# Kernel tuning notes

Measured on AMD Instinct MI355X. Metric: run time of the kernel, lower is better.

The kernel has to match this reference:

```python
import jax, jax.numpy as jnp
import numpy as np

N_EMBD = 768
N_HEAD = 12
HEAD_DIM = N_EMBD // N_HEAD
B = 4
L_MAIN = 1024
L_SIDE = 1024
HALF = L_SIDE // 2  # occurrences of each modality per row
LN_EPS = 1e-5


def setup_inputs() -> dict:
    key = jax.random.key(0)
    ks = jax.random.split(key, 16)
    x = jax.random.normal(ks[0], (B, L_MAIN, N_EMBD), jnp.float32)
    # ages in years, sorted per-row (events arrive in time order), all >= 0
    age = jnp.sort(jax.random.uniform(ks[1], (B, L_MAIN), jnp.float32) * 80.0, axis=1)
    mod_age = jnp.sort(jax.random.uniform(ks[2], (B, L_SIDE), jnp.float32) * 80.0, axis=1)
    # each row holds exactly HALF tokens of modality 2 and HALF of modality 3, randomly interleaved
    base = jnp.concatenate([jnp.full((HALF,), 2, jnp.int32), jnp.full((HALF,), 3, jnp.int32)])
    mod_idx = jax.vmap(lambda k: jax.random.permutation(k, base))(jax.random.split(ks[3], B))
    mod2_emb = jax.random.normal(ks[4], (B * HALF, N_EMBD), jnp.float32)
    mod3_emb = jax.random.normal(ks[5], (B * HALF, N_EMBD), jnp.float32)

    def lin(k, fan_out, fan_in):
        return 0.02 * jax.random.normal(k, (fan_out, fan_in), jnp.float32)

    params = dict(
        ln0_w=jnp.ones((N_EMBD,), jnp.float32), ln0_b=jnp.zeros((N_EMBD,), jnp.float32),
        ln1_w=jnp.ones((N_EMBD,), jnp.float32), ln1_b=jnp.zeros((N_EMBD,), jnp.float32),
        ln2_w=jnp.ones((N_EMBD,), jnp.float32), ln2_b=jnp.zeros((N_EMBD,), jnp.float32),
        q_w=lin(ks[6], N_EMBD, N_EMBD), q_b=jnp.zeros((N_EMBD,), jnp.float32),
        k_w=lin(ks[7], N_EMBD, N_EMBD), k_b=jnp.zeros((N_EMBD,), jnp.float32),
        v_w=lin(ks[8], N_EMBD, N_EMBD), v_b=jnp.zeros((N_EMBD,), jnp.float32),
        c_w=lin(ks[9], N_EMBD, N_EMBD), c_b=jnp.zeros((N_EMBD,), jnp.float32),
        fc_w=lin(ks[10], 4 * N_EMBD, N_EMBD), fc_b=jnp.zeros((4 * N_EMBD,), jnp.float32),
        proj_w=lin(ks[11], N_EMBD, 4 * N_EMBD), proj_b=jnp.zeros((N_EMBD,), jnp.float32),
    )
    return dict(x=x, age=age, mod_idx=mod_idx, mod_age=mod_age,
                mod2_emb=mod2_emb, mod3_emb=mod3_emb, **params)


def _ln(t, w, b):
    m = jnp.mean(t, axis=-1, keepdims=True)
    v = jnp.var(t, axis=-1, keepdims=True)
    return (t - m) * jax.lax.rsqrt(v + LN_EPS) * w + b


def _fuse_embed(mod_idx, mod_age, mod2_emb, mod3_emb):
    # torch: stable argsort by age, then scatter each modality's embeddings into
    # its matching positions in row-major nonzero order.
    order = jnp.argsort(mod_age, axis=1, stable=True)
    s_idx = jnp.take_along_axis(mod_idx, order, axis=1)  # [B, L_side]
    rows = jnp.arange(s_idx.shape[0])[:, None]
    def scatter_mod(val, m_emb):
        mask = s_idx == val
        occ = jnp.cumsum(mask, axis=1) - 1          # per-row occurrence counter
        gidx = rows * HALF + jnp.clip(occ, 0, HALF - 1)  # global row-major index
        return jnp.where(mask[..., None], m_emb[gidx], 0.0)
    return scatter_mod(2, mod2_emb) + scatter_mod(3, mod3_emb)


def _cross_fusion(x, age, mod_idx, mod_age, mod2_emb, mod3_emb,
                  ln0_w, ln0_b, ln1_w, ln1_b, ln2_w, ln2_b,
                  q_w, q_b, k_w, k_b, v_w, v_b, c_w, c_b,
                  fc_w, fc_b, proj_w, proj_b):
    mod_x = _fuse_embed(mod_idx, mod_age, mod2_emb, mod3_emb)  # [B, L_side, E]
    # time_attention_mask: query may attend to keys with key_age <= query_age, pad = key_age >= 0
    attn_mask = (age[:, :, None] >= mod_age[:, None, :]) & (mod_age >= 0.0)[:, None, :]
    attn_mask = attn_mask[:, None, :, :]  # [B, 1, L_main, L_side]

    xn = _ln(x, ln1_w, ln1_b)
    sn = _ln(mod_x, ln0_w, ln0_b)
    q = (xn @ q_w.T + q_b).reshape(B, L_MAIN, N_HEAD, HEAD_DIM).transpose(0, 2, 1, 3)
    k = (sn @ k_w.T + k_b).reshape(B, L_SIDE, N_HEAD, HEAD_DIM).transpose(0, 2, 1, 3)
    v = (sn @ v_w.T + v_b).reshape(B, L_SIDE, N_HEAD, HEAD_DIM).transpose(0, 2, 1, 3)

    att = jnp.einsum('bhqd,bhkd->bhqk', q, k) * (HEAD_DIM ** -0.5)
    all_masked = ~jnp.any(attn_mask, axis=-1, keepdims=True)
    # fully-masked rows: use 0 logits (uniform softmax) then zero out -> matches
    # torch's masked_fill(all_masked, 0) after nan softmax, but grad-safe.
    neg = jnp.where(all_masked, 0.0, -jnp.inf)
    att = jnp.where(attn_mask, att, neg)
    att = jax.nn.softmax(att, axis=-1)
    att = jnp.where(all_masked, 0.0, att)

    y = jnp.einsum('bhqk,bhkd->bhqd', att, v)
    y = y.transpose(0, 2, 1, 3).reshape(B, L_MAIN, N_EMBD)
    x = x + (y @ c_w.T + c_b)
    h = _ln(x, ln2_w, ln2_b)
    h = jax.nn.gelu(h @ fc_w.T + fc_b, approximate=False)
    x = x + (h @ proj_w.T + proj_b)
    return x


def reference(x, age, mod_idx, mod_age, mod2_emb, mod3_emb,
              ln0_w, ln0_b, ln1_w, ln1_b, ln2_w, ln2_b,
              q_w, q_b, k_w, k_b, v_w, v_b, c_w, c_b,
              fc_w, fc_b, proj_w, proj_b):
    return _cross_fusion(x, age, mod_idx, mod_age, mod2_emb, mod3_emb,
                         ln0_w, ln0_b, ln1_w, ln1_b, ln2_w, ln2_b,
                         q_w, q_b, k_w, k_b, v_w, v_b, c_w, c_b,
                         fc_w, fc_b, proj_w, proj_b)
```

## Files before the change

### kernel.cpp

```cpp
#include <hip/hip_runtime.h>

#define N_EMBD 768
#define SEQ    1024
#define NBATCH 4
#define NHEAD  12
#define HDIM   64
#define NROWS  4096
#define FFN    3072
#define W768   589824
#define WFC    2359296
#define NCVT   6912

typedef unsigned short u16;
typedef __bf16 bf16x8 __attribute__((ext_vector_type(8)));
typedef float  f32x4  __attribute__((ext_vector_type(4)));
typedef unsigned short u16x8 __attribute__((ext_vector_type(8)));

typedef const __attribute__((address_space(1))) unsigned int gu32;
typedef __attribute__((address_space(3))) unsigned int lu32;
#define GLL(g, l) __builtin_amdgcn_global_load_lds((gu32*)(g), (lu32*)(l), 16, 0, 0)

__device__ __forceinline__ u16 f2bf(float f) {
    union { float f; unsigned int i; } v; v.f = f;
    unsigned int r = v.i + 0x7fffu + ((v.i >> 16) & 1u);
    return (u16)(r >> 16);
}

__global__ __launch_bounds__(256) void prep_kernel(const float* __restrict__ qw,
                                                   const float* __restrict__ kw,
                                                   const float* __restrict__ vw,
                                                   const float* __restrict__ cw,
                                                   const float* __restrict__ fcw,
                                                   const float* __restrict__ pw,
                                                   u16* __restrict__ wdst,
                                                   const float* __restrict__ x,
                                                   const float* __restrict__ ln1w,
                                                   const float* __restrict__ ln1b,
                                                   u16* __restrict__ xn,
                                                   const int* __restrict__ mod_idx,
                                                   int* __restrict__ g) {
    int bx = blockIdx.x;
    if (bx < NCVT) {
        size_t e = ((size_t)bx * 256 + threadIdx.x) * 4;
        const float* src; size_t base;
        if      (e < 1 * (size_t)W768) { src = qw;  base = 0; }
        else if (e < 2 * (size_t)W768) { src = kw;  base = 1 * (size_t)W768; }
        else if (e < 3 * (size_t)W768) { src = vw;  base = 2 * (size_t)W768; }
        else if (e < 4 * (size_t)W768) { src = cw;  base = 3 * (size_t)W768; }
        else if (e < 4 * (size_t)W768 + WFC) { src = fcw; base = 4 * (size_t)W768; }
        else { src = pw; base = 4 * (size_t)W768 + WFC; }
        float4 v = *(const float4*)(src + (e - base));
        ushort4 o;
        o.x = f2bf(v.x); o.y = f2bf(v.y); o.z = f2bf(v.z); o.w = f2bf(v.w);
        *(ushort4*)(wdst + e) = o;
    } else if (bx < NCVT + 1024) {
        int row  = (bx - NCVT) * 4 + (threadIdx.x >> 6);
        int lane = threadIdx.x & 63;
        const float* p = x + (size_t)row * N_EMBD;
        float vals[12];
        float s = 0.f, sq = 0.f;
#pragma unroll
        for (int c = 0; c < 12; c++) {
            float v = p[c * 64 + lane];
            vals[c] = v; s += v; sq += v * v;
        }
#pragma unroll
        for (int o = 32; o > 0; o >>= 1) { s += __shfl_xor(s, o); sq += __shfl_xor(sq, o); }
        float mean = s * (1.0f / 768.0f);
        float var  = sq * (1.0f / 768.0f) - mean * mean;
        float r    = rsqrtf(var + 1e-5f);
        u16* d = xn + (size_t)row * N_EMBD;
#pragma unroll
        for (int c = 0; c < 12; c++) {
            int idx = c * 64 + lane;
            d[idx] = f2bf((vals[c] - mean) * r * ln1w[idx] + ln1b[idx]);
        }
    } else {
        __shared__ int sc[256];
        int b = bx - NCVT - 1024;
        int j = threadIdx.x;
        int4 mi = *(const int4*)(mod_idx + b * SEQ + j * 4);
        int f0 = (mi.x == 2), f1 = (mi.y == 2), f2v = (mi.z == 2), f3 = (mi.w == 2);
        int t1 = f0 + f1, t2 = t1 + f2v, t3 = t2 + f3;
        sc[j] = t3;
        __syncthreads();
        for (int off = 1; off < 256; off <<= 1) {
            int add = (j >= off) ? sc[j - off] : 0;
            __syncthreads();
            sc[j] += add;
            __syncthreads();
        }
        int excl = sc[j] - t3;
        int cin[4] = {excl + f0, excl + t1, excl + t2, excl + t3};
        int fl[4] = {f0, f1, f2v, f3};
#pragma unroll
        for (int i2 = 0; i2 < 4; i2++) {
            int jj = j * 4 + i2;
            int occ = fl[i2] ? (cin[i2] - 1) : (jj - cin[i2]);
            occ = occ < 0 ? 0 : (occ > 511 ? 511 : occ);
            g[b * SEQ + jj] = fl[i2] ? (b * 512 + occ) : (2048 + b * 512 + occ);
        }
    }
}

__global__ __launch_bounds__(256) void ln_rows(const float* __restrict__ src,
                                               const float* __restrict__ src2,
                                               const int* __restrict__ g,
                                               const float* __restrict__ w,
                                               const float* __restrict__ b,
                                               u16* __restrict__ dst) {
    int row  = blockIdx.x * 4 + (threadIdx.x >> 6);
    int lane = threadIdx.x & 63;
    const float* p;
    if (g) {
        int gi = g[row];
        p = (gi < 2048) ? (src + (size_t)gi * N_EMBD)
                        : (src2 + (size_t)(gi - 2048) * N_EMBD);
    } else {
        p = src + (size_t)row * N_EMBD;
    }
    float vals[12];
    float s = 0.f, sq = 0.f;
#pragma unroll
    for (int c = 0; c < 12; c++) {
        float v = p[c * 64 + lane];
        vals[c] = v; s += v; sq += v * v;
    }
#pragma unroll
    for (int o = 32; o > 0; o >>= 1) { s += __shfl_xor(s, o); sq += __shfl_xor(sq, o); }
    float mean = s * (1.0f / 768.0f);
    float var  = sq * (1.0f / 768.0f) - mean * mean;
    float r    = rsqrtf(var + 1e-5f);
    u16* d = dst + (size_t)row * N_EMBD;
#pragma unroll
    for (int c = 0; c < 12; c++) {
        int idx = c * 64 + lane;
        d[idx] = f2bf((vals[c] - mean) * r * w[idx] + b[idx]);
    }
}

__device__ __forceinline__ void core128(const u16* __restrict__ A, const u16* __restrict__ W,
                                        int K, int m0, int n0, int t,
                                        u16* As, u16* Bs, f32x4 (&acc)[4][4]) {
    int w = t >> 6, lane = t & 63, quad = lane >> 4, l16 = lane & 15;
    int r16 = lane >> 2, c8 = (lane & 3) * 8;
    int wm = (w >> 1) * 64, wn = (w & 1) * 64;
    for (int k0 = 0; k0 < K; k0 += 32) {
        __syncthreads();
        const u16* ga = A + (size_t)(m0 + w * 32 + r16) * K + k0 + c8;
        const u16* gb = W + (size_t)(n0 + w * 32 + r16) * K + k0 + c8;
        GLL(ga,                  &As[(w * 32) * 32]);
        GLL(ga + 16 * (size_t)K, &As[(w * 32 + 16) * 32]);
        GLL(gb,                  &Bs[(w * 32) * 32]);
        GLL(gb + 16 * (size_t)K, &Bs[(w * 32 + 16) * 32]);
        __syncthreads();
        bf16x8 af[4], bfr[4];
#pragma unroll
        for (int i = 0; i < 4; i++)
            af[i] = *(const bf16x8*)&As[(wm + i * 16 + l16) * 32 + quad * 8];
#pragma unroll
        for (int j = 0; j < 4; j++)
            bfr[j] = *(const bf16x8*)&Bs[(wn + j * 16 + l16) * 32 + quad * 8];
#pragma unroll
        for (int i = 0; i < 4; i++)
#pragma unroll
            for (int j = 0; j < 4; j++)
                acc[i][j] = __builtin_amdgcn_mfma_f32_16x16x32_bf16(af[i], bfr[j], acc[i][j], 0, 0, 0);
    }
}

__device__ __forceinline__ void core64(const u16* __restrict__ A, const u16* __restrict__ W,
                                       int K, int kBeg, int kEnd, int m0, int n0, int t,
                                       u16* As, u16* Bs, f32x4 (&acc)[2][4]) {
    int w = t >> 6, lane = t & 63, quad = lane >> 4, l16 = lane & 15;
    int r16 = lane >> 2, c8 = (lane & 3) * 8;
    int wm = (w >> 1) * 32, wn = (w & 1) * 64;
    for (int k0 = kBeg; k0 < kEnd; k0 += 32) {
        __syncthreads();
        const u16* gb = W + (size_t)(n0 + w * 32 + r16) * K + k0 + c8;
        GLL(A + (size_t)(m0 + w * 16 + r16) * K + k0 + c8, &As[(w * 16) * 32]);
        GLL(gb,                  &Bs[(w * 32) * 32]);
        GLL(gb + 16 * (size_t)K, &Bs[(w * 32 + 16) * 32]);
        __syncthreads();
        bf16x8 af[2], bfr[4];
#pragma unroll
        for (int i = 0; i < 2; i++)
            af[i] = *(const bf16x8*)&As[(wm + i * 16 + l16) * 32 + quad * 8];
#pragma unroll
        for (int j = 0; j < 4; j++)
            bfr[j] = *(const bf16x8*)&Bs[(wn + j * 16 + l16) * 32 + quad * 8];
#pragma unroll
        for (int i = 0; i < 2; i++)
#pragma unroll
            for (int j = 0; j < 4; j++)
                acc[i][j] = __builtin_amdgcn_mfma_f32_16x16x32_bf16(af[i], bfr[j], acc[i][j], 0, 0, 0);
    }
}

__global__ __launch_bounds__(256) void gemm_qkv(const u16* __restrict__ xn,
                                                const u16* __restrict__ sn,
                                                const u16* __restrict__ wq,
                                                const float* __restrict__ qb,
                                                const float* __restrict__ kb,
                                                const float* __restrict__ vb,
                                                u16* __restrict__ outbase) {
    __shared__ u16 As[128 * 32], Bs[128 * 32];
    int z = blockIdx.z;
    const u16* A = (z == 0) ? xn : sn;
    const u16* W = wq + (size_t)z * W768;
    const float* bias = (z == 0) ? qb : ((z == 1) ? kb : vb);
    u16* C = outbase + (size_t)z * ((size_t)NROWS * N_EMBD);
    int m0 = blockIdx.y * 128, n0 = blockIdx.x * 128;
    int t = threadIdx.x;
    f32x4 acc[4][4];
#pragma unroll
    for (int i = 0; i < 4; i++)
#pragma unroll
        for (int j = 0; j < 4; j++) acc[i][j] = (f32x4){0.f, 0.f, 0.f, 0.f};
    core128(A, W, N_EMBD, m0, n0, t, As, Bs, acc);
    int w = t >> 6, lane = t & 63, quad = lane >> 4, l16 = lane & 15;
    int wm = (w >> 1) * 64, wn = (w & 1) * 64;
#pragma unroll
    for (int j = 0; j < 4; j++) {
        int col = n0 + wn + j * 16 + l16;
        float bv = bias[col];
#pragma unroll
        for (int i = 0; i < 4; i++) {
            int rowb = m0 + wm + i * 16 + quad * 4;
#pragma unroll
            for (int r = 0; r < 4; r++)
                C[(size_t)(rowb + r) * N_EMBD + col] = f2bf(acc[i][j][r] + bv);
        }
    }
}

__global__ __launch_bounds__(256) void gemm_fc(const u16* __restrict__ A,
                                               const u16* __restrict__ W,
                                               const float* __restrict__ bias,
                                               u16* __restrict__ C) {
    __shared__ u16 As[128 * 32], Bs[128 * 32];
    int m0 = blockIdx.y * 128, n0 = blockIdx.x * 128;
    int t = threadIdx.x;
    f32x4 acc[4][4];
#pragma unroll
    for (int i = 0; i < 4; i++)
#pragma unroll
        for (int j = 0; j < 4; j++) acc[i][j] = (f32x4){0.f, 0.f, 0.f, 0.f};
    core128(A, W, N_EMBD, m0, n0, t, As, Bs, acc);
    int w = t >> 6, lane = t & 63, quad = lane >> 4, l16 = lane & 15;
    int wm = (w >> 1) * 64, wn = (w & 1) * 64;
#pragma unroll
    for (int j = 0; j < 4; j++) {
        int col = n0 + wn + j * 16 + l16;
        float bv = bias[col];
#pragma unroll
        for (int i = 0; i < 4; i++) {
            int rowb = m0 + wm + i * 16 + quad * 4;
#pragma unroll
            for (int r = 0; r < 4; r++) {
                float v = acc[i][j][r] + bv;
                float y = v * (1.595769122f + 0.071354816f * v * v);
                float gel = v / (1.0f + __expf(-y));
                C[(size_t)(rowb + r) * FFN + col] = f2bf(gel);
            }
        }
    }
}

__global__ __launch_bounds__(256) void gemm_cproj(const u16* __restrict__ A,
                                                  const u16* __restrict__ W,
                                                  const float* __restrict__ bias,
                                                  const float* __restrict__ Res,
                                                  float* __restrict__ C) {
    __shared__ u16 As[64 * 32], Bs[128 * 32];
    int m0 = blockIdx.y * 64, n0 = blockIdx.x * 128;
    int t = threadIdx.x;
    f32x4 acc[2][4];
#pragma unroll
    for (int i = 0; i < 2; i++)
#pragma unroll
        for (int j = 0; j < 4; j++) acc[i][j] = (f32x4){0.f, 0.f, 0.f, 0.f};
    core64(A, W, N_EMBD, 0, N_EMBD, m0, n0, t, As, Bs, acc);
    int w = t >> 6, lane = t & 63, quad = lane >> 4, l16 = lane & 15;
    int wm = (w >> 1) * 32, wn = (w & 1) * 64;
#pragma unroll
    for (int j = 0; j < 4; j++) {
        int col = n0 + wn + j * 16 + l16;
        float bv = bias[col];
#pragma unroll
        for (int i = 0; i < 2; i++) {
            int rowb = m0 + wm + i * 16 + quad * 4;
#pragma unroll
            for (int r = 0; r < 4; r++) {
                size_t idx = (size_t)(rowb + r) * N_EMBD + col;
                C[idx] = acc[i][j][r] + bv + Res[idx];
            }
        }
    }
}

__global__ __launch_bounds__(256) void gemm_proj_split(const u16* __restrict__ A,
                                                       const u16* __restrict__ W,
                                                       float* __restrict__ p0,
                                                       float* __restrict__ p1) {
    __shared__ u16 As[64 * 32], Bs[128 * 32];
    int z = blockIdx.z;
    float* P = z ? p1 : p0;
    int m0 = blockIdx.y * 64, n0 = blockIdx.x * 128;
    int t = threadIdx.x;
    f32x4 acc[2][4];
#pragma unroll
    for (int i = 0; i < 2; i++)
#pragma unroll
        for (int j = 0; j < 4; j++) acc[i][j] = (f32x4){0.f, 0.f, 0.f, 0.f};
    core64(A, W, FFN, z * (FFN / 2), (z + 1) * (FFN / 2), m0, n0, t, As, Bs, acc);
    int w = t >> 6, lane = t & 63, quad = lane >> 4, l16 = lane & 15;
    int wm = (w >> 1) * 32, wn = (w & 1) * 64;
#pragma unroll
    for (int j = 0; j < 4; j++) {
        int col = n0 + wn + j * 16 + l16;
#pragma unroll
        for (int i = 0; i < 2; i++) {
            int rowb = m0 + wm + i * 16 + quad * 4;
#pragma unroll
            for (int r = 0; r < 4; r++)
                P[(size_t)(rowb + r) * N_EMBD + col] = acc[i][j][r];
        }
    }
}

__global__ __launch_bounds__(256) void reduce_proj(const float* __restrict__ p0,
                                                   const float* __restrict__ p1,
                                                   const float* __restrict__ bias,
                                                   const float* __restrict__ x1,
                                                   float* __restrict__ out) {
    size_t idx = ((size_t)blockIdx.x * 256 + threadIdx.x) * 4;
    int col = (int)(idx % N_EMBD);
    float4 a = *(const float4*)(p0 + idx);
    float4 b = *(const float4*)(p1 + idx);
    float4 r = *(const float4*)(x1 + idx);
    float4 bb = *(const float4*)(bias + col);
    float4 o;
    o.x = a.x + b.x + r.x + bb.x;
    o.y = a.y + b.y + r.y + bb.y;
    o.z = a.z + b.z + r.z + bb.z;
    o.w = a.w + b.w + r.w + bb.w;
    *(float4*)(out + idx) = o;
}

#define KST 72

__global__ __launch_bounds__(256) void attn_kernel(const u16* __restrict__ Q,
                                                   const u16* __restrict__ K,
                                                   const u16* __restrict__ V,
                                                   const float* __restrict__ age,
                                                   const float* __restrict__ mod_age,
                                                   u16* __restrict__ Y) {
    __shared__ u16 Kl[64 * KST];
    __shared__ u16 Vt[64 * KST];
    __shared__ u16 Pl[4][16 * KST];

    int bx = blockIdx.x;
    int qt = 15 - (bx / 48);
    int bh = bx % 48;
    int b = bh / NHEAD, h = bh % NHEAD;
    int t = threadIdx.x;
    int w = t >> 6, lane = t & 63, quad = lane >> 4, l16 = lane & 15;
    int q0 = qt * 64 + w * 16;

    size_t qrowbase = ((size_t)(b * SEQ + q0 + l16)) * N_EMBD + h * HDIM;
    bf16x8 qf0 = *(const bf16x8*)&Q[qrowbase + quad * 8];
    bf16x8 qf1 = *(const bf16x8*)&Q[qrowbase + 32 + quad * 8];

    float age_r[4];
#pragma unroll
    for (int r = 0; r < 4; r++) age_r[r] = age[b * SEQ + q0 + quad * 4 + r];
    float age_q0      = __shfl(age_r[0], 0);
    float age_max_blk = age[b * SEQ + qt * 64 + 63];
    float mod_min     = mod_age[b * SEQ];

    float mv0 = (lane < 16) ? mod_age[b * SEQ + lane * 64] : 1e30f;
    unsigned long long bm = __ballot(mv0 > age_max_blk);
    int nkt = bm ? (__ffsll(bm) - 1) : 16;

    int krow0 = t >> 3,        kc8 = (t & 7) * 8;
    int krow1 = 32 + (t >> 3);
    int vrow  = t & 63;
    int vc8_0 = t >> 6, vc8_1 = 4 + (t >> 6);

    float m_i[4] = {-1e30f, -1e30f, -1e30f, -1e30f};
    float l_i[4] = {0.f, 0.f, 0.f, 0.f};
    f32x4 o[4];
#pragma unroll
    for (int nt = 0; nt < 4; nt++) o[nt] = (f32x4){0.f, 0.f, 0.f, 0.f};

    u16x8 kr0, kr1, vr0, vr1;
    float mreg = 0.f;
    if (nkt > 0) {
        size_t kb = ((size_t)(b * SEQ)) * N_EMBD + h * HDIM;
        kr0 = *(const u16x8*)(K + kb + (size_t)krow0 * N_EMBD + kc8);
        kr1 = *(const u16x8*)(K + kb + (size_t)krow1 * N_EMBD + kc8);
        vr0 = *(const u16x8*)(V + kb + (size_t)vrow * N_EMBD + vc8_0 * 8);
        vr1 = *(const u16x8*)(V + kb + (size_t)vrow * N_EMBD + vc8_1 * 8);
        mreg = mod_age[b * SEQ + lane];
    }

    for (int kt = 0; kt < nkt; kt++) {
        __syncthreads();
        *(u16x8*)&Kl[krow0 * KST + kc8] = kr0;
        *(u16x8*)&Kl[krow1 * KST + kc8] = kr1;
#pragma unroll
        for (int e = 0; e < 8; e++) Vt[(vc8_0 * 8 + e) * KST + vrow] = vr0[e];
#pragma unroll
        for (int e = 0; e < 8; e++) Vt[(vc8_1 * 8 + e) * KST + vrow] = vr1[e];
        float mcur = mreg;
        __syncthreads();

        if (kt + 1 < nkt) {
            size_t kb = ((size_t)(b * SEQ + (kt + 1) * 64)) * N_EMBD + h * HDIM;
            kr0 = *(const u16x8*)(K + kb + (size_t)krow0 * N_EMBD + kc8);
            kr1 = *(const u16x8*)(K + kb + (size_t)krow1 * N_EMBD + kc8);
            vr0 = *(const u16x8*)(V + kb + (size_t)vrow * N_EMBD + vc8_0 * 8);
            vr1 = *(const u16x8*)(V + kb + (size_t)vrow * N_EMBD + vc8_1 * 8);
            mreg = mod_age[b * SEQ + (kt + 1) * 64 + lane];
        }

        float tile_max = __shfl(mcur, 63);
        bool need_mask = tile_max > age_q0;
        float p[4][4];
#pragma unroll
        for (int jt = 0; jt < 4; jt++) {
            f32x4 s = (f32x4){0.f, 0.f, 0.f, 0.f};
            bf16x8 kf0 = *(const bf16x8*)&Kl[(jt * 16 + l16) * KST + quad * 8];
            bf16x8 kf1 = *(const bf16x8*)&Kl[(jt * 16 + l16) * KST + 32 + quad * 8];
            s = __builtin_amdgcn_mfma_f32_16x16x32_bf16(qf0, kf0, s, 0, 0, 0);
            s = __builtin_amdgcn_mfma_f32_16x16x32_bf16(qf1, kf1, s, 0, 0, 0);
            float mval = __shfl(mcur, jt * 16 + l16);
#pragma unroll
            for (int r = 0; r < 4; r++) {
                float sv = s[r] * 0.125f;
                p[jt][r] = (!need_mask || mval <= age_r[r]) ? sv : -1e30f;
            }
        }
        float alpha[4];
#pragma unroll
        for (int r = 0; r < 4; r++) {
            float mx = fmaxf(fmaxf(p[0][r], p[1][r]), fmaxf(p[2][r], p[3][r]));
#pragma unroll
            for (int msk = 1; msk < 16; msk <<= 1) mx = fmaxf(mx, __shfl_xor(mx, msk));
            float mnew = fmaxf(m_i[r], mx);
            alpha[r] = __expf(m_i[r] - mnew);
            float srow = 0.f;
#pragma unroll
            for (int jt = 0; jt < 4; jt++) {
                float pv = __expf(p[jt][r] - mnew);
                p[jt][r] = pv;
                srow += pv;
            }
#pragma unroll
            for (int msk = 1; msk < 16; msk <<= 1) srow += __shfl_xor(srow, msk);
            l_i[r] = l_i[r] * alpha[r] + srow;
            m_i[r] = mnew;
        }
#pragma unroll
        for (int jt = 0; jt < 4; jt++)
#pragma unroll
            for (int r = 0; r < 4; r++)
                Pl[w][(quad * 4 + r) * KST + jt * 16 + l16] = f2bf(p[jt][r]);
#pragma unroll
        for (int nt = 0; nt < 4; nt++)
#pragma unroll
            for (int r = 0; r < 4; r++) o[nt][r] *= alpha[r];
#pragma unroll
        for (int c = 0; c < 2; c++) {
            bf16x8 pf = *(const bf16x8*)&Pl[w][l16 * KST + c * 32 + quad * 8];
#pragma unroll
            for (int nt = 0; nt < 4; nt++) {
                bf16x8 vf = *(const bf16x8*)&Vt[(nt * 16 + l16) * KST + c * 32 + quad * 8];
                o[nt] = __builtin_amdgcn_mfma_f32_16x16x32_bf16(pf, vf, o[nt], 0, 0, 0);
            }
        }
    }
#pragma unroll
    for (int r = 0; r < 4; r++) {
        int qrow = q0 + quad * 4 + r;
        float inv = (age_r[r] >= mod_min) ? (1.0f / l_i[r]) : 0.0f;
#pragma unroll
        for (int nt = 0; nt < 4; nt++)
            Y[((size_t)(b * SEQ + qrow)) * N_EMBD + h * HDIM + nt * 16 + l16] =
                f2bf(o[nt][r] * inv);
    }
}

extern "C" void kernel_launch(void* const* d_in, const int* in_sizes, int n_in,
                              void* d_out, int out_size, void* d_ws, size_t ws_size,
                              hipStream_t stream) {
    const float* x       = (const float*)d_in[0];
    const float* age     = (const float*)d_in[1];
    const int*   mod_idx = (const int*)d_in[2];
    const float* mod_age = (const float*)d_in[3];
    const float* mod2    = (const float*)d_in[4];
    const float* mod3    = (const float*)d_in[5];
    const float* ln0w = (const float*)d_in[6],  *ln0b = (const float*)d_in[7];
    const float* ln1w = (const float*)d_in[8],  *ln1b = (const float*)d_in[9];
    const float* ln2w = (const float*)d_in[10], *ln2b = (const float*)d_in[11];
    const float* qb = (const float*)d_in[13];
    const float* kb = (const float*)d_in[15];
    const float* vb = (const float*)d_in[17];
    const float* cb = (const float*)d_in[19];
    const float* fcb = (const float*)d_in[21];
    const float* pb = (const float*)d_in[23];

    char* ws = (char*)d_ws;
    const size_t RB = (size_t)NROWS * N_EMBD * 2;
    int* g   = (int*)ws;
    u16* wq  = (u16*)(ws + 32768);
    u16* wc  = wq + 3 * (size_t)W768;
    u16* wfc = wq + 4 * (size_t)W768;
    u16* wp  = wq + 4 * (size_t)W768 + WFC;
    size_t off = 32768 + 2 * (4 * (size_t)W768 + 2 * (size_t)WFC);
    u16* xn   = (u16*)(ws + off); off += RB;
    u16* sn   = (u16*)(ws + off); off += RB;
    u16* qbuf = (u16*)(ws + off); off += RB;
    u16* kbuf = (u16*)(ws + off); off += RB;
    u16* vbuf = (u16*)(ws + off); off += RB;
    float* x1 = (float*)(ws + off); off += (size_t)NROWS * N_EMBD * 4;
    u16* hbuf = (u16*)(ws + off);
    u16* yb = xn;  u16* hn = qbuf;
    float* p0 = (float*)xn;
    float* p1 = (float*)kbuf;

    prep_kernel<<<NCVT + 1024 + NBATCH, 256, 0, stream>>>(
        (const float*)d_in[12], (const float*)d_in[14], (const float*)d_in[16],
        (const float*)d_in[18], (const float*)d_in[20], (const float*)d_in[22], wq,
        x, ln1w, ln1b, xn, mod_idx, g);
    ln_rows<<<NROWS / 4, 256, 0, stream>>>(mod2, mod3, g, ln0w, ln0b, sn);

    gemm_qkv<<<dim3(N_EMBD / 128, NROWS / 128, 3), 256, 0, stream>>>(xn, sn, wq, qb, kb, vb, qbuf);

    attn_kernel<<<NBATCH * NHEAD * 16, 256, 0, stream>>>(qbuf, kbuf, vbuf, age, mod_age, yb);

    gemm_cproj<<<dim3(N_EMBD / 128, NROWS / 64), 256, 0, stream>>>(yb, wc, cb, x, x1);
    ln_rows<<<NROWS / 4, 256, 0, stream>>>(x1, nullptr, nullptr, ln2w, ln2b, hn);
    gemm_fc<<<dim3(FFN / 128, NROWS / 128), 256, 0, stream>>>(hn, wfc, fcb, hbuf);
    gemm_proj_split<<<dim3(N_EMBD / 128, NROWS / 64, 2), 256, 0, stream>>>(hbuf, wp, p0, p1);
    reduce_proj<<<(NROWS * N_EMBD / 4) / 256, 256, 0, stream>>>(p0, p1, pb, x1, (float*)d_out);

    (void)in_sizes; (void)n_in; (void)out_size; (void)ws_size;
}
```

Measured before the change: 307.1 us.

## Shrink GEMM tiles to 64 rows and add split-K to c-proj and proj

The QKV and FC GEMMs switch from 128x128 tiles to 64x128 tiles, which doubles the number of blocks. The c-proj GEMM becomes a 2-way split-K. Its partial sums, bias and residual are added inside a new fused LN2 kernel that also writes x1. The proj GEMM goes from 2-way to 3-way split-K, with the third partial written straight into the output and added in the reduce step. The aim is better CU occupancy on a device with many CUs, and removing one LN pass over x1. The cost is more global traffic for partial buffers and less reuse per tile.

```diff
diff --git a/kernel.cpp b/kernel.cpp
--- a/kernel.cpp
+++ b/kernel.cpp
@@ -139,33 +139,36 @@
     }
 }
 
-__device__ __forceinline__ void core128(const u16* __restrict__ A, const u16* __restrict__ W,
-                                        int K, int m0, int n0, int t,
-                                        u16* As, u16* Bs, f32x4 (&acc)[4][4]) {
-    int w = t >> 6, lane = t & 63, quad = lane >> 4, l16 = lane & 15;
-    int r16 = lane >> 2, c8 = (lane & 3) * 8;
-    int wm = (w >> 1) * 64, wn = (w & 1) * 64;
-    for (int k0 = 0; k0 < K; k0 += 32) {
-        __syncthreads();
-        const u16* ga = A + (size_t)(m0 + w * 32 + r16) * K + k0 + c8;
-        const u16* gb = W + (size_t)(n0 + w * 32 + r16) * K + k0 + c8;
-        GLL(ga,                  &As[(w * 32) * 32]);
-        GLL(ga + 16 * (size_t)K, &As[(w * 32 + 16) * 32]);
-        GLL(gb,                  &Bs[(w * 32) * 32]);
-        GLL(gb + 16 * (size_t)K, &Bs[(w * 32 + 16) * 32]);
-        __syncthreads();
-        bf16x8 af[4], bfr[4];
-#pragma unroll
-        for (int i = 0; i < 4; i++)
-            af[i] = *(const bf16x8*)&As[(wm + i * 16 + l16) * 32 + quad * 8];
-#pragma unroll
-        for (int j = 0; j < 4; j++)
-            bfr[j] = *(const bf16x8*)&Bs[(wn + j * 16 + l16) * 32 + quad * 8];
-#pragma unroll
-        for (int i = 0; i < 4; i++)
-#pragma unroll
-            for (int j = 0; j < 4; j++)
-                acc[i][j] = __builtin_amdgcn_mfma_f32_16x16x32_bf16(af[i], bfr[j], acc[i][j], 0, 0, 0);
+__global__ __launch_bounds__(256) void ln2_fused(const float* __restrict__ pa,
+                                                 const float* __restrict__ pb,
+                                                 const float* __restrict__ cb,
+                                                 const float* __restrict__ x,
+                                                 const float* __restrict__ ln2w,
+                                                 const float* __restrict__ ln2b,
+                                                 float* __restrict__ x1,
+                                                 u16* __restrict__ hn) {
+    int row  = blockIdx.x * 4 + (threadIdx.x >> 6);
+    int lane = threadIdx.x & 63;
+    size_t base = (size_t)row * N_EMBD;
+    float vals[12];
+    float s = 0.f, sq = 0.f;
+#pragma unroll
+    for (int c = 0; c < 12; c++) {
+        int idx = c * 64 + lane;
+        float v = pa[base + idx] + pb[base + idx] + cb[idx] + x[base + idx];
+        vals[c] = v; s += v; sq += v * v;
+        x1[base + idx] = v;
+    }
+#pragma unroll
+    for (int o = 32; o > 0; o >>= 1) { s += __shfl_xor(s, o); sq += __shfl_xor(sq, o); }
+    float mean = s * (1.0f / 768.0f);
+    float var  = sq * (1.0f / 768.0f) - mean * mean;
+    float r    = rsqrtf(var + 1e-5f);
+    u16* d = hn + base;
+#pragma unroll
+    for (int c = 0; c < 12; c++) {
+        int idx = c * 64 + lane;
+        d[idx] = f2bf((vals[c] - mean) * r * ln2w[idx] + ln2b[idx]);
     }
 }
 
@@ -204,28 +207,28 @@
                                                 const float* __restrict__ kb,
                                                 const float* __restrict__ vb,
                                                 u16* __restrict__ outbase) {
-    __shared__ u16 As[128 * 32], Bs[128 * 32];
+    __shared__ u16 As[64 * 32], Bs[128 * 32];
     int z = blockIdx.z;
     const u16* A = (z == 0) ? xn : sn;
     const u16* W = wq + (size_t)z * W768;
     const float* bias = (z == 0) ? qb : ((z == 1) ? kb : vb);
     u16* C = outbase + (size_t)z * ((size_t)NROWS * N_EMBD);
-    int m0 = blockIdx.y * 128, n0 = blockIdx.x * 128;
+    int m0 = blockIdx.y * 64, n0 = blockIdx.x * 128;
     int t = threadIdx.x;
-    f32x4 acc[4][4];
-#pragma unroll
-    for (int i = 0; i < 4; i++)
+    f32x4 acc[2][4];
+#pragma unroll
+    for (int i = 0; i < 2; i++)
 #pragma unroll
         for (int j = 0; j < 4; j++) acc[i][j] = (f32x4){0.f, 0.f, 0.f, 0.f};
-    core128(A, W, N_EMBD, m0, n0, t, As, Bs, acc);
+    core64(A, W, N_EMBD, 0, N_EMBD, m0, n0, t, As, Bs, acc);
     int w = t >> 6, lane = t & 63, quad = lane >> 4, l16 = lane & 15;
-    int wm = (w >> 1) * 64, wn = (w & 1) * 64;
+    int wm = (w >> 1) * 32, wn = (w & 1) * 64;
 #pragma unroll
     for (int j = 0; j < 4; j++) {
         int col = n0 + wn + j * 16 + l16;
         float bv = bias[col];
 #pragma unroll
-        for (int i = 0; i < 4; i++) {
+        for (int i = 0; i < 2; i++) {
             int rowb = m0 + wm + i * 16 + quad * 4;
 #pragma unroll
             for (int r = 0; r < 4; r++)
@@ -238,23 +241,23 @@
                                                const u16* __restrict__ W,
                                                const float* __restrict__ bias,
                                                u16* __restrict__ C) {
-    __shared__ u16 As[128 * 32], Bs[128 * 32];
-    int m0 = blockIdx.y * 128, n0 = blockIdx.x * 128;
+    __shared__ u16 As[64 * 32], Bs[128 * 32];
+    int m0 = blockIdx.y * 64, n0 = blockIdx.x * 128;
     int t = threadIdx.x;
-    f32x4 acc[4][4];
-#pragma unroll
-    for (int i = 0; i < 4; i++)
+    f32x4 acc[2][4];
+#pragma unroll
+    for (int i = 0; i < 2; i++)
 #pragma unroll
         for (int j = 0; j < 4; j++) acc[i][j] = (f32x4){0.f, 0.f, 0.f, 0.f};
-    core128(A, W, N_EMBD, m0, n0, t, As, Bs, acc);
+    core64(A, W, N_EMBD, 0, N_EMBD, m0, n0, t, As, Bs, acc);
     int w = t >> 6, lane = t & 63, quad = lane >> 4, l16 = lane & 15;
-    int wm = (w >> 1) * 64, wn = (w & 1) * 64;
+    int wm = (w >> 1) * 32, wn = (w & 1) * 64;
 #pragma unroll
     for (int j = 0; j < 4; j++) {
         int col = n0 + wn + j * 16 + l16;
         float bv = bias[col];
 #pragma unroll
-        for (int i = 0; i < 4; i++) {
+        for (int i = 0; i < 2; i++) {
             int rowb = m0 + wm + i * 16 + quad * 4;
 #pragma unroll
             for (int r = 0; r < 4; r++) {
@@ -267,12 +270,13 @@
     }
 }
 
-__global__ __launch_bounds__(256) void gemm_cproj(const u16* __restrict__ A,
-                                                  const u16* __restrict__ W,
-                                                  const float* __restrict__ bias,
-                                                  const float* __restrict__ Res,
-                                                  float* __restrict__ C) {
+__global__ __launch_bounds__(256) void gemm_cproj_split(const u16* __restrict__ A,
+                                                        const u16* __restrict__ W,
+                                                        float* __restrict__ pa,
+                                                        float* __restrict__ pb) {
     __shared__ u16 As[64 * 32], Bs[128 * 32];
+    int z = blockIdx.z;
+    float* P = z ? pb : pa;
     int m0 = blockIdx.y * 64, n0 = blockIdx.x * 128;
     int t = threadIdx.x;
     f32x4 acc[2][4];
@@ -280,21 +284,18 @@
     for (int i = 0; i < 2; i++)
 #pragma unroll
         for (int j = 0; j < 4; j++) acc[i][j] = (f32x4){0.f, 0.f, 0.f, 0.f};
-    core64(A, W, N_EMBD, 0, N_EMBD, m0, n0, t, As, Bs, acc);
+    core64(A, W, N_EMBD, z * 384, (z + 1) * 384, m0, n0, t, As, Bs, acc);
     int w = t >> 6, lane = t & 63, quad = lane >> 4, l16 = lane & 15;
     int wm = (w >> 1) * 32, wn = (w & 1) * 64;
 #pragma unroll
     for (int j = 0; j < 4; j++) {
         int col = n0 + wn + j * 16 + l16;
-        float bv = bias[col];
 #pragma unroll
         for (int i = 0; i < 2; i++) {
             int rowb = m0 + wm + i * 16 + quad * 4;
 #pragma unroll
-            for (int r = 0; r < 4; r++) {
-                size_t idx = (size_t)(rowb + r) * N_EMBD + col;
-                C[idx] = acc[i][j][r] + bv + Res[idx];
-            }
+            for (int r = 0; r < 4; r++)
+                P[(size_t)(rowb + r) * N_EMBD + col] = acc[i][j][r];
         }
     }
 }
@@ -302,10 +303,11 @@
 __global__ __launch_bounds__(256) void gemm_proj_split(const u16* __restrict__ A,
                                                        const u16* __restrict__ W,
                                                        float* __restrict__ p0,
-                                                       float* __restrict__ p1) {
+                                                       float* __restrict__ p1,
+                                                       float* __restrict__ p2) {
     __shared__ u16 As[64 * 32], Bs[128 * 32];
     int z = blockIdx.z;
-    float* P = z ? p1 : p0;
+    float* P = (z == 0) ? p0 : ((z == 1) ? p1 : p2);
     int m0 = blockIdx.y * 64, n0 = blockIdx.x * 128;
     int t = threadIdx.x;
     f32x4 acc[2][4];
@@ -313,7 +315,7 @@
     for (int i = 0; i < 2; i++)
 #pragma unroll
         for (int j = 0; j < 4; j++) acc[i][j] = (f32x4){0.f, 0.f, 0.f, 0.f};
-    core64(A, W, FFN, z * (FFN / 2), (z + 1) * (FFN / 2), m0, n0, t, As, Bs, acc);
+    core64(A, W, FFN, z * 1024, (z + 1) * 1024, m0, n0, t, As, Bs, acc);
     int w = t >> 6, lane = t & 63, quad = lane >> 4, l16 = lane & 15;
     int wm = (w >> 1) * 32, wn = (w & 1) * 64;
 #pragma unroll
@@ -338,13 +340,14 @@
     int col = (int)(idx % N_EMBD);
     float4 a = *(const float4*)(p0 + idx);
     float4 b = *(const float4*)(p1 + idx);
+    float4 c = *(const float4*)(out + idx);
     float4 r = *(const float4*)(x1 + idx);
     float4 bb = *(const float4*)(bias + col);
     float4 o;
-    o.x = a.x + b.x + r.x + bb.x;
-    o.y = a.y + b.y + r.y + bb.y;
-    o.z = a.z + b.z + r.z + bb.z;
-    o.w = a.w + b.w + r.w + bb.w;
+    o.x = a.x + b.x + c.x + r.x + bb.x;
+    o.y = a.y + b.y + c.y + r.y + bb.y;
+    o.z = a.z + b.z + c.z + r.z + bb.z;
+    o.w = a.w + b.w + c.w + r.w + bb.w;
     *(float4*)(out + idx) = o;
 }
 
@@ -518,17 +521,21 @@
     u16* wc  = wq + 3 * (size_t)W768;
     u16* wfc = wq + 4 * (size_t)W768;
     u16* wp  = wq + 4 * (size_t)W768 + WFC;
-    size_t off = 32768 + 2 * (4 * (size_t)W768 + 2 * (size_t)WFC);
-    u16* xn   = (u16*)(ws + off); off += RB;
-    u16* sn   = (u16*)(ws + off); off += RB;
-    u16* qbuf = (u16*)(ws + off); off += RB;
-    u16* kbuf = (u16*)(ws + off); off += RB;
-    u16* vbuf = (u16*)(ws + off); off += RB;
-    float* x1 = (float*)(ws + off); off += (size_t)NROWS * N_EMBD * 4;
-    u16* hbuf = (u16*)(ws + off);
-    u16* yb = xn;  u16* hn = qbuf;
-    float* p0 = (float*)xn;
-    float* p1 = (float*)kbuf;
+    size_t actoff = 32768 + 2 * (4 * (size_t)W768 + 2 * (size_t)WFC);
+    char* act = ws + actoff;
+    u16* xn   = (u16*)(act);
+    u16* sn   = (u16*)(act + RB);
+    u16* qbuf = (u16*)(act + 2 * RB);
+    u16* kbuf = (u16*)(act + 3 * RB);
+    u16* vbuf = (u16*)(act + 4 * RB);
+    float* x1 = (float*)(act + 5 * RB);
+    u16* hbuf = (u16*)(act + 5 * RB + (size_t)NROWS * N_EMBD * 4);
+    u16* yb = xn;
+    float* cpa = (float*)(act + RB);
+    float* cpb = (float*)(act + 3 * RB);
+    u16* hn = xn;
+    float* pp0 = (float*)(act);
+    float* pp1 = (float*)(act + 2 * RB);
 
     prep_kernel<<<NCVT + 1024 + NBATCH, 256, 0, stream>>>(
         (const float*)d_in[12], (const float*)d_in[14], (const float*)d_in[16],
@@ -536,15 +543,15 @@
         x, ln1w, ln1b, xn, mod_idx, g);
     ln_rows<<<NROWS / 4, 256, 0, stream>>>(mod2, mod3, g, ln0w, ln0b, sn);
 
-    gemm_qkv<<<dim3(N_EMBD / 128, NROWS / 128, 3), 256, 0, stream>>>(xn, sn, wq, qb, kb, vb, qbuf);
+    gemm_qkv<<<dim3(N_EMBD / 128, NROWS / 64, 3), 256, 0, stream>>>(xn, sn, wq, qb, kb, vb, qbuf);
 
     attn_kernel<<<NBATCH * NHEAD * 16, 256, 0, stream>>>(qbuf, kbuf, vbuf, age, mod_age, yb);
 
-    gemm_cproj<<<dim3(N_EMBD / 128, NROWS / 64), 256, 0, stream>>>(yb, wc, cb, x, x1);
-    ln_rows<<<NROWS / 4, 256, 0, stream>>>(x1, nullptr, nullptr, ln2w, ln2b, hn);
-    gemm_fc<<<dim3(FFN / 128, NROWS / 128), 256, 0, stream>>>(hn, wfc, fcb, hbuf);
-    gemm_proj_split<<<dim3(N_EMBD / 128, NROWS / 64, 2), 256, 0, stream>>>(hbuf, wp, p0, p1);
-    reduce_proj<<<(NROWS * N_EMBD / 4) / 256, 256, 0, stream>>>(p0, p1, pb, x1, (float*)d_out);
+    gemm_cproj_split<<<dim3(N_EMBD / 128, NROWS / 64, 2), 256, 0, stream>>>(yb, wc, cpa, cpb);
+    ln2_fused<<<NROWS / 4, 256, 0, stream>>>(cpa, cpb, cb, x, ln2w, ln2b, x1, hn);
+    gemm_fc<<<dim3(FFN / 128, NROWS / 64), 256, 0, stream>>>(hn, wfc, fcb, hbuf);
+    gemm_proj_split<<<dim3(N_EMBD / 128, NROWS / 64, 3), 256, 0, stream>>>(hbuf, wp, pp0, pp1, (float*)d_out);
+    reduce_proj<<<(NROWS * N_EMBD / 4) / 256, 256, 0, stream>>>(pp0, pp1, pb, x1, (float*)d_out);
 
     (void)in_sizes; (void)n_in; (void)out_size; (void)ws_size;
 }
```

New measurement: 329.7 us. 7.4% more time.
